# Performance work log

Hardware: AMD Instinct MI355X
Metric: run time of the kernel (lower is better)

The kernel has to match this reference:

```python
import jax, jax.numpy as jnp
import numpy as np

# D4 Daubechies filter taps (same filter replicated across all channels)
D4 = jnp.array([0.4829629131445341, 0.8365163037378079, 0.2241438680420134, -0.1294095225512604], dtype=jnp.float32)
N_SCALES = 11
SPARSE_DILATIONS = (512, 1024)


def setup_inputs() -> dict:
    key = jax.random.key(0)
    ks = jax.random.split(key, 12)
    B, N, D, H = 4, 4096, 1024, 16
    s = 0.02
    return {
        "x": jax.random.normal(ks[0], (B, N, D), dtype=jnp.float32),
        "Wqkv": jax.random.normal(ks[1], (D, 3 * D), dtype=jnp.float32) * s,
        "bqkv": jnp.zeros((3 * D,), dtype=jnp.float32),
        "Wout": jax.random.normal(ks[2], (D, D), dtype=jnp.float32) * s,
        "bout": jnp.zeros((D,), dtype=jnp.float32),
        "Wgate": jax.random.normal(ks[3], (D, D), dtype=jnp.float32) * s,
        "bgate": jnp.full((D,), 2.0, dtype=jnp.float32),  # nn.init.constant_(bias, 2.0)
        "scale_gain": jax.random.normal(ks[4], (N_SCALES, H), dtype=jnp.float32) * 0.1,
        "skip_w": jnp.full((len(SPARSE_DILATIONS),), -4.0, dtype=jnp.float32)
                  + jax.random.normal(ks[5], (len(SPARSE_DILATIONS),), dtype=jnp.float32) * 0.1,
        "coupling": jnp.eye(H, dtype=jnp.float32)
                    + 0.01 * jax.random.normal(ks[6], (H, H), dtype=jnp.float32),
    }


def _shift_right(t, s, N):
    """Causal shift along seq axis (axis=2): out[i] = t[i-s], zeros for i < s."""
    if s == 0:
        return t
    return jnp.pad(t, ((0, 0), (0, 0), (s, 0), (0, 0)))[:, :, :N, :]


def reference(x, Wqkv, bqkv, Wout, bout, Wgate, bgate, scale_gain, skip_w, coupling):
    B, N, D = x.shape
    H = scale_gain.shape[1]
    HD = D // H

    qkv = x @ Wqkv + bqkv                       # [B, N, 3D]
    q, k, v = jnp.split(qkv, 3, axis=-1)

    def to_heads(t):
        return t.reshape(B, N, H, HD).transpose(0, 2, 1, 3)  # [B, H, N, HD]

    q, k, v = to_heads(q), to_heads(k), to_heads(v)

    k_mag = jnp.linalg.norm(k, axis=-1, keepdims=True)       # [B, H, N, 1]
    field = v * k_mag                                        # [B, H, N, HD]

    # --- 11-scale causal D4 dilated depthwise conv pyramid ---
    # Depthwise conv with identical filter on every channel == weighted sum of
    # causally shifted copies: y[n] = sum_t D4[t] * field[n - (3-t)*d]
    gains = jax.nn.softmax(scale_gain, axis=0)               # [S, H]
    acc = jnp.zeros_like(field)
    for j in range(scale_gain.shape[0]):
        d = 1 << j
        y = sum(D4[t] * _shift_right(field, (3 - t) * d, N) for t in range(4))
        acc = acc + gains[j][None, :, None, None] * y
    field = acc

    # --- sparse long-distance causal skips (1-tap copies at d=512, 1024) ---
    sw = jax.nn.sigmoid(skip_w)
    skip = sum(sw[i] * _shift_right(field, d, N) for i, d in enumerate(SPARSE_DILATIONS))
    field = field + skip

    # --- gated field coupling across heads ---
    coup = jax.nn.softmax(coupling, axis=-1)                 # [H, H]
    field = jnp.einsum('ij,bjnd->bind', coup, field)

    q_flat = q.transpose(0, 2, 1, 3).reshape(B, N, D)
    gate = jax.nn.sigmoid(q_flat @ Wgate + bgate)
    gathered = field.transpose(0, 2, 1, 3).reshape(B, N, D)
    out = (gathered * gate) @ Wout + bout                    # dropout = identity (eval)
    return out
```

## Files before the change

kernel.cpp:

```cpp
#include <hip/hip_runtime.h>
#include <hip/hip_bf16.h>
#include <math.h>

#define BB 4
#define NSEQ 4096
#define DD 1024
#define HH 16
#define HD 64
#define MROWS (BB * NSEQ)

typedef __attribute__((ext_vector_type(8))) short short8;
typedef float v4f __attribute__((ext_vector_type(4)));
typedef unsigned short u16;

typedef __attribute__((address_space(1))) const void gconst_void;
typedef __attribute__((address_space(3))) void lds_void_t;

__device__ __constant__ int SHIFTS[24] = {0,1,2,3,4,6,8,12,16,24,32,48,64,96,128,192,256,384,512,768,1024,1536,2048,3072};

__device__ inline u16 f2bf(float f) {
    unsigned u = __float_as_uint(f);
    unsigned r = u + 0x7fffu + ((u >> 16) & 1u);
    return (u16)(r >> 16);
}
__device__ inline float bf2f(u16 h) {
    return __uint_as_float(((unsigned)h) << 16);
}
__device__ inline void gl2lds16(const u16* g, u16* l) {
    __builtin_amdgcn_global_load_lds((gconst_void*)g, (lds_void_t*)l, 16, 0, 0);
}

__global__ void prep_kernel(const float* __restrict__ scale_gain, const float* __restrict__ skip_w,
                            const float* __restrict__ coupling, float* __restrict__ coefTab,
                            float* __restrict__ coupS, float* __restrict__ swbuf) {
    const float D4T[4] = {0.4829629131445341f, 0.8365163037378079f, 0.2241438680420134f, -0.1294095225512604f};
    int t = threadIdx.x;
    if (t < 2) swbuf[t] = 1.0f / (1.0f + expf(-skip_w[t]));
    if (t < 16) {
        float m = -1e30f;
        for (int j = 0; j < 16; j++) m = fmaxf(m, coupling[t * 16 + j]);
        float s = 0.f, e[16];
        for (int j = 0; j < 16; j++) { e[j] = expf(coupling[t * 16 + j] - m); s += e[j]; }
        for (int j = 0; j < 16; j++) coupS[t * 16 + j] = e[j] / s;
        float g[11];
        m = -1e30f;
        for (int j = 0; j < 11; j++) m = fmaxf(m, scale_gain[j * 16 + t]);
        s = 0.f;
        for (int j = 0; j < 11; j++) { g[j] = expf(scale_gain[j * 16 + t] - m); s += g[j]; }
        for (int j = 0; j < 11; j++) g[j] /= s;
        float cf[24];
        for (int i = 0; i < 24; i++) cf[i] = 0.f;
        for (int j = 0; j < 11; j++) {
            int d = 1 << j;
            for (int tt = 0; tt < 4; tt++) {
                int sh = (3 - tt) * d;
                for (int i = 0; i < 24; i++) {
                    if (SHIFTS[i] == sh) { cf[i] += g[j] * D4T[tt]; break; }
                }
            }
        }
        for (int i = 0; i < 24; i++) coefTab[t * 24 + i] = cf[i];
    }
}

__global__ __launch_bounds__(256) void bfuse_kernel(const float* __restrict__ bqkv, const float* __restrict__ Wgate,
                                                    const float* __restrict__ bgate, float* __restrict__ bfuse) {
    __shared__ float part[4][64];
    int nloc = threadIdx.x & 63, strip = threadIdx.x >> 6;
    int n = blockIdx.x * 64 + nloc;
    float s = 0.f;
    for (int j = strip * 256; j < strip * 256 + 256; j++)
        s += bqkv[j] * Wgate[(long)j * 1024 + n];
    part[strip][nloc] = s;
    __syncthreads();
    if (strip == 0)
        bfuse[n] = bgate[n] + part[0][nloc] + part[1][nloc] + part[2][nloc] + part[3][nloc];
}

__global__ __launch_bounds__(256) void cast_x_kernel(const float* __restrict__ x, u16* __restrict__ xb) {
    long i = ((long)blockIdx.x * 256 + threadIdx.x) * 8;
    float4 f0 = *(const float4*)&x[i];
    float4 f1 = *(const float4*)&x[i + 4];
    u16 o[8];
    o[0] = f2bf(f0.x); o[1] = f2bf(f0.y); o[2] = f2bf(f0.z); o[3] = f2bf(f0.w);
    o[4] = f2bf(f1.x); o[5] = f2bf(f1.y); o[6] = f2bf(f1.z); o[7] = f2bf(f1.w);
    *(uint4*)&xb[i] = *(uint4*)o;
}

__global__ __launch_bounds__(256) void transpose_cast(const float* __restrict__ W, long ldw,
                                                      u16* __restrict__ WT, long ldt) {
    __shared__ float tile[32][33];
    int tx = threadIdx.x, ty = threadIdx.y;
    long x = (long)blockIdx.x * 32 + tx;
    long y0 = (long)blockIdx.y * 32;
    for (int r = 0; r < 32; r += 8)
        tile[ty + r][tx] = W[(y0 + ty + r) * ldw + x];
    __syncthreads();
    for (int r = 0; r < 32; r += 8)
        WT[((long)blockIdx.x * 32 + ty + r) * ldt + y0 + tx] = f2bf(tile[tx][ty + r]);
}

__global__ __launch_bounds__(256) void cast_q_kernel(const float* __restrict__ Wqkv, u16* __restrict__ WqC) {
    long i = ((long)blockIdx.x * 256 + threadIdx.x) * 4;
    int row = (int)(i >> 10);
    int col = (int)(i & 1023);
    float4 f = *(const float4*)&Wqkv[(long)row * 3072 + col];
    ushort4 o;
    o.x = f2bf(f.x); o.y = f2bf(f.y); o.z = f2bf(f.z); o.w = f2bf(f.w);
    *(ushort4*)&WqC[i] = o;
}

__global__ __launch_bounds__(256) void gemm64(const u16* __restrict__ A, long lda,
                                              const u16* __restrict__ BT, long ldb, int K,
                                              u16* __restrict__ C, long ldc) {
    __shared__ u16 As[64 * 32];
    __shared__ u16 Bs[64 * 32];
    const int tid = threadIdx.x;
    const int wv = tid >> 6, lane = tid & 63;
    const int wm = wv >> 1, wn = wv & 1;
    const int lrow = lane & 15, kq = lane >> 4;
    const long m0 = (long)blockIdx.y * 64, n0 = (long)blockIdx.x * 64;

    const int srow = wv * 16 + (lane >> 2);
    const int scol = ((lane & 3) ^ ((lane >> 3) & 3)) * 8;
    const u16* gA = A + (m0 + srow) * lda + scol;
    const u16* gB = BT + (n0 + srow) * ldb + scol;
    u16* la = &As[wv * 16 * 32];
    u16* lb = &Bs[wv * 16 * 32];

    const int acol = (kq ^ ((lrow >> 1) & 3)) * 8;
    v4f acc[2][2];
#pragma unroll
    for (int i = 0; i < 2; i++)
#pragma unroll
        for (int j = 0; j < 2; j++) acc[i][j] = (v4f){0.f, 0.f, 0.f, 0.f};

    for (int k0 = 0; k0 < K; k0 += 32) {
        gl2lds16(gA + k0, la);
        gl2lds16(gB + k0, lb);
        __syncthreads();
        short8 af[2], bf[2];
#pragma unroll
        for (int i = 0; i < 2; i++) af[i] = *(const short8*)&As[(wm * 32 + i * 16 + lrow) * 32 + acol];
#pragma unroll
        for (int j = 0; j < 2; j++) bf[j] = *(const short8*)&Bs[(wn * 32 + j * 16 + lrow) * 32 + acol];
#pragma unroll
        for (int im = 0; im < 2; im++)
#pragma unroll
            for (int in = 0; in < 2; in++)
                acc[im][in] = __builtin_amdgcn_mfma_f32_16x16x32_bf16(af[im], bf[in], acc[im][in], 0, 0, 0);
        __syncthreads();
    }
#pragma unroll
    for (int im = 0; im < 2; im++) {
#pragma unroll
        for (int in = 0; in < 2; in++) {
            long row = m0 + wm * 32 + im * 16 + kq * 4;
            long col = n0 + wn * 32 + in * 16 + lrow;
#pragma unroll
            for (int i = 0; i < 4; i++)
                C[(row + i) * ldc + col] = f2bf(acc[im][in][i]);
        }
    }
}

#define WAITV(N) asm volatile("s_waitcnt vmcnt(" #N ")" ::: "memory")

template <int CMODE>
__global__ __launch_bounds__(512, 2) void gemm256(const u16* __restrict__ A, long lda,
                                                  const u16* __restrict__ BT, long ldb, int K,
                                                  const float* __restrict__ bias,
                                                  const float* __restrict__ bias2,
                                                  void* __restrict__ C0, void* __restrict__ C1,
                                                  long ldc, float* __restrict__ kmagOut) {
    __shared__ u16 smem[4 * 2 * 8192];
    const int tid = threadIdx.x;
    const int wv = tid >> 6, lane = tid & 63;
    const int wm = wv >> 2, wn = wv & 3;
    const int lrow = lane & 15, kq = lane >> 4;
    const long m0 = (long)blockIdx.y * 256, n0 = (long)blockIdx.x * 256;

    const int srow = wv * 32 + (lane >> 2);
    const int scol = ((lane & 3) ^ ((lane >> 3) & 3)) * 8;
    const u16* gA0 = A + (m0 + srow) * lda + scol;
    const u16* gA1 = gA0 + 16 * lda;
    const u16* gB0 = BT + (n0 + srow) * ldb + scol;
    const u16* gB1 = gB0 + 16 * ldb;
    const int sb = wv * 32 * 32;

    const int acol = (kq ^ ((lrow >> 1) & 3)) * 8;
    const int aoff = (wm * 128 + lrow) * 32 + acol;
    const int boff = (wn * 64 + lrow) * 32 + acol;

    v4f acc[8][4];
#pragma unroll
    for (int i = 0; i < 8; i++)
#pragma unroll
        for (int j = 0; j < 4; j++) acc[i][j] = (v4f){0.f, 0.f, 0.f, 0.f};

    const int NT = K >> 5;

#define STAGE256(tt) {                                              \
        const int _kk = (tt) << 5;                                  \
        u16* _p = &smem[(((tt) & 3) * 2) * 8192 + sb];              \
        gl2lds16(gA0 + _kk, _p);                                    \
        gl2lds16(gA1 + _kk, _p + 512);                              \
        gl2lds16(gB0 + _kk, _p + 8192);                             \
        gl2lds16(gB1 + _kk, _p + 8192 + 512); }

    STAGE256(0)
    STAGE256(1)
    STAGE256(2)
    WAITV(8);
    __builtin_amdgcn_s_barrier();

    for (int t = 0; t < NT; ++t) {
        if (t + 3 < NT) STAGE256(t + 3)
        const u16* Ab = &smem[((t & 3) * 2) * 8192];
        const u16* Bb = Ab + 8192;
        short8 af[8], bf[4];
#pragma unroll
        for (int i = 0; i < 8; i++) af[i] = *(const short8*)&Ab[aoff + i * 512];
#pragma unroll
        for (int j = 0; j < 4; j++) bf[j] = *(const short8*)&Bb[boff + j * 512];
        __builtin_amdgcn_s_setprio(1);
#pragma unroll
        for (int i = 0; i < 8; i++)
#pragma unroll
            for (int j = 0; j < 4; j++)
                acc[i][j] = __builtin_amdgcn_mfma_f32_16x16x32_bf16(af[i], bf[j], acc[i][j], 0, 0, 0);
        __builtin_amdgcn_s_setprio(0);
        if (t + 3 < NT)      { WAITV(8); }
        else if (t + 2 < NT) { WAITV(4); }
        else if (t + 1 < NT) { WAITV(0); }
        __builtin_amdgcn_s_barrier();
    }
#undef STAGE256

    if (CMODE == 0) {
        float* C = (float*)C0;
#pragma unroll
        for (int im = 0; im < 8; im++) {
#pragma unroll
            for (int in = 0; in < 4; in++) {
                long row = m0 + wm * 128 + im * 16 + kq * 4;
                long col = n0 + wn * 64 + in * 16 + lrow;
                float bv = bias ? bias[col] : 0.f;
#pragma unroll
                for (int i = 0; i < 4; i++)
                    C[(row + i) * ldc + col] = acc[im][in][i] + bv;
            }
        }
    } else {
        u16* kvC = (u16*)C0;
        u16* gateC = (u16*)C1;
        const bool isGate = (n0 >= 2048);
        if (isGate) {
#pragma unroll
            for (int im = 0; im < 8; im++) {
#pragma unroll
                for (int in = 0; in < 4; in++) {
                    long row = m0 + wm * 128 + im * 16 + kq * 4;
                    long gc = n0 + wn * 64 + in * 16 + lrow - 2048;
                    float bv = bias2[gc];
#pragma unroll
                    for (int i = 0; i < 4; i++) {
                        float sgm = 1.0f / (1.0f + expf(-(acc[im][in][i] + bv)));
                        gateC[(row + i) * 1024 + gc] = f2bf(sgm);
                    }
                }
            }
        } else if (n0 < 1024) {
            float bvv[4];
#pragma unroll
            for (int in = 0; in < 4; in++) bvv[in] = bias[n0 + wn * 64 + in * 16 + lrow];
            const int h_g = (int)(n0 >> 6) + wn;
#pragma unroll
            for (int im = 0; im < 8; im++) {
                long row = m0 + wm * 128 + im * 16 + kq * 4;
                float ss0 = 0.f, ss1 = 0.f, ss2 = 0.f, ss3 = 0.f;
#pragma unroll
                for (int in = 0; in < 4; in++) {
                    long col = n0 + wn * 64 + in * 16 + lrow;
                    float v0 = acc[im][in][0] + bvv[in];
                    float v1 = acc[im][in][1] + bvv[in];
                    float v2 = acc[im][in][2] + bvv[in];
                    float v3 = acc[im][in][3] + bvv[in];
                    kvC[(row + 0) * 2048 + col] = f2bf(v0);
                    kvC[(row + 1) * 2048 + col] = f2bf(v1);
                    kvC[(row + 2) * 2048 + col] = f2bf(v2);
                    kvC[(row + 3) * 2048 + col] = f2bf(v3);
                    ss0 += v0 * v0; ss1 += v1 * v1; ss2 += v2 * v2; ss3 += v3 * v3;
                }
#pragma unroll
                for (int m = 1; m <= 8; m <<= 1) {
                    ss0 += __shfl_xor(ss0, m, 64);
                    ss1 += __shfl_xor(ss1, m, 64);
                    ss2 += __shfl_xor(ss2, m, 64);
                    ss3 += __shfl_xor(ss3, m, 64);
                }
                if (lrow == 0) {
                    int b = (int)(row >> 12);
                    int n = (int)(row & 4095);
                    float4 o4 = make_float4(sqrtf(ss0), sqrtf(ss1), sqrtf(ss2), sqrtf(ss3));
                    *(float4*)&kmagOut[((long)b * HH + h_g) * NSEQ + n] = o4;
                }
            }
        } else {
#pragma unroll
            for (int im = 0; im < 8; im++) {
#pragma unroll
                for (int in = 0; in < 4; in++) {
                    long row = m0 + wm * 128 + im * 16 + kq * 4;
                    long col = n0 + wn * 64 + in * 16 + lrow;
                    float bv = bias[col];
#pragma unroll
                    for (int i = 0; i < 4; i++)
                        kvC[(row + i) * 2048 + col] = f2bf(acc[im][in][i] + bv);
                }
            }
        }
    }
}

__global__ __launch_bounds__(256) void foldv_kernel(const u16* __restrict__ kv,
                                                    const float* __restrict__ kmag,
                                                    u16* __restrict__ field_t) {
    __shared__ u16 tile[64][72];
    int bh = blockIdx.y;
    int n0 = blockIdx.x * 64;
    int b = bh >> 4, h = bh & 15;
    int t = threadIdx.x;

    {
        int r = t >> 2;
        int c0 = (t & 3) * 16;
        int n = n0 + r;
        const u16* src = kv + ((long)(b * NSEQ + n)) * 2048 + 1024 + h * 64 + c0;
        uint4 u0 = *(const uint4*)src;
        uint4 u1 = *(const uint4*)(src + 8);
        float km = kmag[(long)bh * NSEQ + n];
        u16 in[16], o[16];
        *(uint4*)&in[0] = u0;
        *(uint4*)&in[8] = u1;
#pragma unroll
        for (int i = 0; i < 16; i++) o[i] = f2bf(bf2f(in[i]) * km);
        *(uint4*)&tile[r][c0] = *(uint4*)&o[0];
        *(uint4*)&tile[r][c0 + 8] = *(uint4*)&o[8];
    }
    __syncthreads();

    {
        int cg = t >> 4;
        int q = t & 15;
        u16 o[16];
#pragma unroll
        for (int j = 0; j < 4; j++) {
            int r = q * 4 + j;
            *(ushort4*)&o[j * 4] = *(const ushort4*)&tile[r][cg * 4];
        }
        u16* dst = field_t + (((long)bh * 16 + cg) * NSEQ + n0 + q * 4) * 4;
        *(uint4*)&dst[0] = *(uint4*)&o[0];
        *(uint4*)&dst[8] = *(uint4*)&o[8];
    }
}

__global__ __launch_bounds__(512) void pyramid_kernel(const u16* __restrict__ field_t,
                                                      const float* __restrict__ coefTab,
                                                      const float* __restrict__ swbuf,
                                                      u16* __restrict__ accp) {
    __shared__ u16 lds4[NSEQ * 4];
    int blk = blockIdx.x;
    int bh = blk >> 4;
    int cg = blk & 15;
    int hd0 = cg * 4;
    int h = bh & 15;
    int tid = threadIdx.x;

    float cf[24];
#pragma unroll
    for (int i = 0; i < 24; i++) cf[i] = coefTab[h * 24 + i];
    float sw0 = swbuf[0], sw1 = swbuf[1];

    const u16* src = field_t + ((long)bh * 16 + cg) * NSEQ * 4;
#pragma unroll
    for (int k = 0; k < 4; k++) {
        long e = ((long)k * 512 + tid) * 8;
        *(uint4*)&lds4[e] = *(const uint4*)&src[e];
    }
    __syncthreads();

    u16* dst = accp + (long)bh * NSEQ * HD + hd0;
    float p1x = 0.f, p1y = 0.f, p1z = 0.f, p1w = 0.f;
    float p2x = 0.f, p2y = 0.f, p2z = 0.f, p2w = 0.f;
    for (int i = 0; i < 8; i++) {
        int n = tid + i * 512;
        float ax = 0.f, ay = 0.f, az = 0.f, aw = 0.f;
#pragma unroll
        for (int tp = 0; tp < 24; tp++) {
            int s = SHIFTS[tp];
            if (n >= s) {
                const ushort4 f = *(const ushort4*)&lds4[(n - s) * 4];
                float c = cf[tp];
                ax += c * bf2f(f.x); ay += c * bf2f(f.y);
                az += c * bf2f(f.z); aw += c * bf2f(f.w);
            }
        }
        float ox = ax + sw0 * p1x + sw1 * p2x;
        float oy = ay + sw0 * p1y + sw1 * p2y;
        float oz = az + sw0 * p1z + sw1 * p2z;
        float ow = aw + sw0 * p1w + sw1 * p2w;
        ushort4 o;
        o.x = f2bf(ox); o.y = f2bf(oy); o.z = f2bf(oz); o.w = f2bf(ow);
        *(ushort4*)&dst[(long)n * HD] = o;
        p2x = p1x; p2y = p1y; p2z = p1z; p2w = p1w;
        p1x = ax;  p1y = ay;  p1z = az;  p1w = aw;
    }
}

__global__ __launch_bounds__(256) void couple_kernel(const u16* __restrict__ accp,
                                                     const u16* __restrict__ gate,
                                                     const float* __restrict__ coupS,
                                                     u16* __restrict__ A3) {
    __shared__ float tmp[DD];
    __shared__ float cp[256];
    int row = blockIdx.x;
    int b = row >> 12;
    int n = row & 4095;
    int tid = threadIdx.x;
    cp[tid] = coupS[tid];

    int e = tid * 4;
    int j = e >> 6;
    int hd = e & 63;
    const u16* base = accp + (((long)b * HH + j) * NSEQ + n) * HD + hd;
    ushort4 v0 = *(const ushort4*)base;
    tmp[e] = bf2f(v0.x); tmp[e + 1] = bf2f(v0.y);
    tmp[e + 2] = bf2f(v0.z); tmp[e + 3] = bf2f(v0.w);
    __syncthreads();

    float ox = 0.f, oy = 0.f, oz = 0.f, ow = 0.f;
#pragma unroll
    for (int jj = 0; jj < 16; jj++) {
        float c = cp[j * 16 + jj];
        ox += c * tmp[jj * 64 + hd];
        oy += c * tmp[jj * 64 + hd + 1];
        oz += c * tmp[jj * 64 + hd + 2];
        ow += c * tmp[jj * 64 + hd + 3];
    }
    const ushort4 g = *(const ushort4*)&gate[(long)row * DD + e];
    ox *= bf2f(g.x); oy *= bf2f(g.y); oz *= bf2f(g.z); ow *= bf2f(g.w);
    ushort4 o;
    o.x = f2bf(ox); o.y = f2bf(oy); o.z = f2bf(oz); o.w = f2bf(ow);
    *(ushort4*)&A3[(long)row * DD + e] = o;
}

extern "C" void kernel_launch(void* const* d_in, const int* in_sizes, int n_in,
                              void* d_out, int out_size, void* d_ws, size_t ws_size,
                              hipStream_t stream) {
    const float* x        = (const float*)d_in[0];
    const float* Wqkv     = (const float*)d_in[1];
    const float* bqkv     = (const float*)d_in[2];
    const float* Wout     = (const float*)d_in[3];
    const float* bout     = (const float*)d_in[4];
    const float* Wgate    = (const float*)d_in[5];
    const float* bgate    = (const float*)d_in[6];
    const float* scale_g  = (const float*)d_in[7];
    const float* skip_w   = (const float*)d_in[8];
    const float* coupling = (const float*)d_in[9];

    char* ws = (char*)d_ws;
    size_t off = 0;
    auto alloc = [&](size_t bytes) { char* p = ws + off; off += (bytes + 255) & ~(size_t)255; return p; };

    u16*   kv      = (u16*)alloc((size_t)MROWS * 2048 * 2);
    u16*   gate    = (u16*)alloc((size_t)MROWS * DD * 2);
    u16*   field_t = (u16*)alloc((size_t)BB * HH * NSEQ * HD * 2);
    u16*   WkvT    = (u16*)alloc((size_t)2048 * 1024 * 2);
    u16*   WfuseT  = (u16*)alloc((size_t)1024 * 1024 * 2);
    u16*   WgateT  = (u16*)alloc((size_t)1024 * 1024 * 2);
    u16*   WoutT   = (u16*)alloc((size_t)1024 * 1024 * 2);
    u16*   WqC     = (u16*)alloc((size_t)1024 * 1024 * 2);
    float* kmag    = (float*)alloc((size_t)BB * HH * NSEQ * 4);
    float* bfuse   = (float*)alloc(1024 * 4);
    float* coefT   = (float*)alloc(16 * 24 * 4);
    float* coupS   = (float*)alloc(256 * 4);
    float* swbuf   = (float*)alloc(2 * 4);
    u16*   xb   = field_t;
    u16*   accp = kv;
    u16*   A3   = kv + (size_t)BB * HH * NSEQ * HD;

    cast_x_kernel<<<(MROWS * DD) / (256 * 8), 256, 0, stream>>>(x, xb);

    prep_kernel<<<1, 64, 0, stream>>>(scale_g, skip_w, coupling, coefT, coupS, swbuf);
    bfuse_kernel<<<16, 256, 0, stream>>>(bqkv, Wgate, bgate, bfuse);

    transpose_cast<<<dim3(64, 32), dim3(32, 8), 0, stream>>>(Wqkv + 1024, 3072, WkvT, 1024);
    transpose_cast<<<dim3(32, 32), dim3(32, 8), 0, stream>>>(Wgate, 1024, WgateT, 1024);
    transpose_cast<<<dim3(32, 32), dim3(32, 8), 0, stream>>>(Wout, 1024, WoutT, 1024);
    cast_q_kernel<<<1024, 256, 0, stream>>>(Wqkv, WqC);

    gemm64<<<dim3(16, 16), 256, 0, stream>>>(WgateT, 1024, WqC, 1024, 1024, WfuseT, 1024);

    gemm256<2><<<dim3(12, 64), 512, 0, stream>>>(xb, 1024, WkvT, 1024, 1024,
                                                 bqkv + 1024, bfuse, kv, gate, 0, kmag);

    foldv_kernel<<<dim3(64, 64), 256, 0, stream>>>(kv, kmag, field_t);

    pyramid_kernel<<<BB * HH * 16, 512, 0, stream>>>(field_t, coefT, swbuf, accp);

    couple_kernel<<<MROWS, 256, 0, stream>>>(accp, gate, coupS, A3);

    gemm256<0><<<dim3(4, 64), 512, 0, stream>>>(A3, 1024, WoutT, 1024, 1024,
                                                bout, (const float*)nullptr, (float*)d_out, nullptr,
                                                1024, (float*)nullptr);
}
```

Baseline: 458.1 us.

## Split GEMM main loop into two barrier-synchronized half-phases interleaving loads and MFMAs

Restructures the 256x256 GEMM inner loop into two phases. Each phase reads half the A fragments from LDS, issues half of the next stage's global-to-LDS copies (A, then B), barriers, then runs half the MFMAs. This is a ping-pong style schedule meant to spread memory issue across the iteration and overlap it with matrix math across the two co-resident workgroups. It adds two extra barriers and lgkmcnt waits per iteration, which could add stalls.

```diff
diff --git a/kernel.cpp b/kernel.cpp
--- a/kernel.cpp
+++ b/kernel.cpp
@@ -165,6 +165,7 @@
 }
 
 #define WAITV(N) asm volatile("s_waitcnt vmcnt(" #N ")" ::: "memory")
+#define LGKM0()  asm volatile("s_waitcnt lgkmcnt(0)" ::: "memory")
 
 template <int CMODE>
 __global__ __launch_bounds__(512, 2) void gemm256(const u16* __restrict__ A, long lda,
@@ -200,32 +201,50 @@
 
     const int NT = K >> 5;
 
-#define STAGE256(tt) {                                              \
+#define STAGE_A(tt) {                                               \
         const int _kk = (tt) << 5;                                  \
         u16* _p = &smem[(((tt) & 3) * 2) * 8192 + sb];              \
         gl2lds16(gA0 + _kk, _p);                                    \
-        gl2lds16(gA1 + _kk, _p + 512);                              \
+        gl2lds16(gA1 + _kk, _p + 512); }
+#define STAGE_B(tt) {                                               \
+        const int _kk = (tt) << 5;                                  \
+        u16* _p = &smem[(((tt) & 3) * 2) * 8192 + sb];              \
         gl2lds16(gB0 + _kk, _p + 8192);                             \
         gl2lds16(gB1 + _kk, _p + 8192 + 512); }
 
-    STAGE256(0)
-    STAGE256(1)
-    STAGE256(2)
+    STAGE_A(0) STAGE_B(0)
+    STAGE_A(1) STAGE_B(1)
+    STAGE_A(2) STAGE_B(2)
     WAITV(8);
     __builtin_amdgcn_s_barrier();
 
     for (int t = 0; t < NT; ++t) {
-        if (t + 3 < NT) STAGE256(t + 3)
         const u16* Ab = &smem[((t & 3) * 2) * 8192];
         const u16* Bb = Ab + 8192;
         short8 af[8], bf[4];
 #pragma unroll
-        for (int i = 0; i < 8; i++) af[i] = *(const short8*)&Ab[aoff + i * 512];
+        for (int i = 0; i < 4; i++) af[i] = *(const short8*)&Ab[aoff + i * 512];
 #pragma unroll
         for (int j = 0; j < 4; j++) bf[j] = *(const short8*)&Bb[boff + j * 512];
+        if (t + 3 < NT) STAGE_A(t + 3)
+        __builtin_amdgcn_s_barrier();
+        LGKM0();
         __builtin_amdgcn_s_setprio(1);
 #pragma unroll
-        for (int i = 0; i < 8; i++)
+        for (int i = 0; i < 4; i++)
+#pragma unroll
+            for (int j = 0; j < 4; j++)
+                acc[i][j] = __builtin_amdgcn_mfma_f32_16x16x32_bf16(af[i], bf[j], acc[i][j], 0, 0, 0);
+        __builtin_amdgcn_s_setprio(0);
+        __builtin_amdgcn_s_barrier();
+#pragma unroll
+        for (int i = 4; i < 8; i++) af[i] = *(const short8*)&Ab[aoff + i * 512];
+        if (t + 3 < NT) STAGE_B(t + 3)
+        __builtin_amdgcn_s_barrier();
+        LGKM0();
+        __builtin_amdgcn_s_setprio(1);
+#pragma unroll
+        for (int i = 4; i < 8; i++)
 #pragma unroll
             for (int j = 0; j < 4; j++)
                 acc[i][j] = __builtin_amdgcn_mfma_f32_16x16x32_bf16(af[i], bf[j], acc[i][j], 0, 0, 0);
@@ -235,7 +254,8 @@
         else if (t + 1 < NT) { WAITV(0); }
         __builtin_amdgcn_s_barrier();
     }
-#undef STAGE256
+#undef STAGE_A
+#undef STAGE_B
 
     if (CMODE == 0) {
         float* C = (float*)C0;
```

After: 451.4 us. About the same (-1.5%).

## Merge preprocessing kernels into one launch and swizzle gemm256 block order

Applied to the files above, without the earlier changes.

Seven small preprocessing launches (x cast, weight transposes, Wq cast, bias fusion, softmax/coef prep) are merged into one kernel that dispatches on block index, which removes launch gaps and tail idle time between them. gemm256 also remaps its linear block id so that consecutive workgroups are spread in strides of eight across the grid. The remap is meant to match how the scheduler distributes workgroups across XCDs so each die's L2 sees better A/B tile reuse. The merged kernel carries branch divergence per block and keeps a __syncthreads inside a device helper reached only by some blocks.

```diff
diff --git a/kernel.cpp b/kernel.cpp
--- a/kernel.cpp
+++ b/kernel.cpp
@@ -30,84 +30,99 @@
     __builtin_amdgcn_global_load_lds((gconst_void*)g, (lds_void_t*)l, 16, 0, 0);
 }
 
-__global__ void prep_kernel(const float* __restrict__ scale_gain, const float* __restrict__ skip_w,
-                            const float* __restrict__ coupling, float* __restrict__ coefTab,
-                            float* __restrict__ coupS, float* __restrict__ swbuf) {
-    const float D4T[4] = {0.4829629131445341f, 0.8365163037378079f, 0.2241438680420134f, -0.1294095225512604f};
-    int t = threadIdx.x;
-    if (t < 2) swbuf[t] = 1.0f / (1.0f + expf(-skip_w[t]));
-    if (t < 16) {
-        float m = -1e30f;
-        for (int j = 0; j < 16; j++) m = fmaxf(m, coupling[t * 16 + j]);
-        float s = 0.f, e[16];
-        for (int j = 0; j < 16; j++) { e[j] = expf(coupling[t * 16 + j] - m); s += e[j]; }
-        for (int j = 0; j < 16; j++) coupS[t * 16 + j] = e[j] / s;
-        float g[11];
-        m = -1e30f;
-        for (int j = 0; j < 11; j++) m = fmaxf(m, scale_gain[j * 16 + t]);
-        s = 0.f;
-        for (int j = 0; j < 11; j++) { g[j] = expf(scale_gain[j * 16 + t] - m); s += g[j]; }
-        for (int j = 0; j < 11; j++) g[j] /= s;
-        float cf[24];
-        for (int i = 0; i < 24; i++) cf[i] = 0.f;
-        for (int j = 0; j < 11; j++) {
-            int d = 1 << j;
-            for (int tt = 0; tt < 4; tt++) {
-                int sh = (3 - tt) * d;
-                for (int i = 0; i < 24; i++) {
-                    if (SHIFTS[i] == sh) { cf[i] += g[j] * D4T[tt]; break; }
+__device__ inline void tcast_dev(const float* __restrict__ W, long ldw, u16* __restrict__ WT, long ldt,
+                                 int bx, int by, int tx, int ty, float (*tile)[33]) {
+    long xg = (long)bx * 32 + tx;
+    long y0 = (long)by * 32;
+    for (int r = 0; r < 32; r += 8)
+        tile[ty + r][tx] = W[(y0 + ty + r) * ldw + xg];
+    __syncthreads();
+    for (int r = 0; r < 32; r += 8)
+        WT[((long)bx * 32 + ty + r) * ldt + y0 + tx] = f2bf(tile[tx][ty + r]);
+}
+
+__global__ __launch_bounds__(256) void prep_data_kernel(
+    const float* __restrict__ x, const float* __restrict__ Wqkv,
+    const float* __restrict__ Wgate, const float* __restrict__ Wout,
+    const float* __restrict__ bqkv, const float* __restrict__ bgate,
+    const float* __restrict__ scale_gain, const float* __restrict__ skip_w,
+    const float* __restrict__ coupling,
+    u16* __restrict__ xb, u16* __restrict__ WkvT, u16* __restrict__ WgateT,
+    u16* __restrict__ WoutT, u16* __restrict__ WqC,
+    float* __restrict__ bfuse, float* __restrict__ coefTab,
+    float* __restrict__ coupS, float* __restrict__ swbuf) {
+    __shared__ float tile[32][33];
+    __shared__ float part[4][64];
+    const int bid = blockIdx.x;
+    const int t = threadIdx.x;
+    const int tx = t & 31, ty = t >> 5;
+
+    if (bid < 8192) {
+        long i = ((long)bid * 256 + t) * 8;
+        float4 f0 = *(const float4*)&x[i];
+        float4 f1 = *(const float4*)&x[i + 4];
+        u16 o[8];
+        o[0] = f2bf(f0.x); o[1] = f2bf(f0.y); o[2] = f2bf(f0.z); o[3] = f2bf(f0.w);
+        o[4] = f2bf(f1.x); o[5] = f2bf(f1.y); o[6] = f2bf(f1.z); o[7] = f2bf(f1.w);
+        *(uint4*)&xb[i] = *(uint4*)o;
+    } else if (bid < 10240) {
+        int r = bid - 8192;
+        tcast_dev(Wqkv + 1024, 3072, WkvT, 1024, r & 63, r >> 6, tx, ty, tile);
+    } else if (bid < 11264) {
+        int r = bid - 10240;
+        tcast_dev(Wgate, 1024, WgateT, 1024, r & 31, r >> 5, tx, ty, tile);
+    } else if (bid < 12288) {
+        int r = bid - 11264;
+        tcast_dev(Wout, 1024, WoutT, 1024, r & 31, r >> 5, tx, ty, tile);
+    } else if (bid < 13312) {
+        int r = bid - 12288;
+        long i = ((long)r * 256 + t) * 4;
+        int row = (int)(i >> 10);
+        int col = (int)(i & 1023);
+        float4 f = *(const float4*)&Wqkv[(long)row * 3072 + col];
+        ushort4 o;
+        o.x = f2bf(f.x); o.y = f2bf(f.y); o.z = f2bf(f.z); o.w = f2bf(f.w);
+        *(ushort4*)&WqC[i] = o;
+    } else if (bid < 13328) {
+        int r = bid - 13312;
+        int nloc = t & 63, strip = t >> 6;
+        int n = r * 64 + nloc;
+        float s = 0.f;
+        for (int j = strip * 256; j < strip * 256 + 256; j++)
+            s += bqkv[j] * Wgate[(long)j * 1024 + n];
+        part[strip][nloc] = s;
+        __syncthreads();
+        if (strip == 0)
+            bfuse[n] = bgate[n] + part[0][nloc] + part[1][nloc] + part[2][nloc] + part[3][nloc];
+    } else {
+        const float D4T[4] = {0.4829629131445341f, 0.8365163037378079f, 0.2241438680420134f, -0.1294095225512604f};
+        if (t < 2) swbuf[t] = 1.0f / (1.0f + expf(-skip_w[t]));
+        if (t < 16) {
+            float m = -1e30f;
+            for (int j = 0; j < 16; j++) m = fmaxf(m, coupling[t * 16 + j]);
+            float s = 0.f, e[16];
+            for (int j = 0; j < 16; j++) { e[j] = expf(coupling[t * 16 + j] - m); s += e[j]; }
+            for (int j = 0; j < 16; j++) coupS[t * 16 + j] = e[j] / s;
+            float g[11];
+            m = -1e30f;
+            for (int j = 0; j < 11; j++) m = fmaxf(m, scale_gain[j * 16 + t]);
+            s = 0.f;
+            for (int j = 0; j < 11; j++) { g[j] = expf(scale_gain[j * 16 + t] - m); s += g[j]; }
+            for (int j = 0; j < 11; j++) g[j] /= s;
+            float cf[24];
+            for (int i = 0; i < 24; i++) cf[i] = 0.f;
+            for (int j = 0; j < 11; j++) {
+                int d = 1 << j;
+                for (int tt = 0; tt < 4; tt++) {
+                    int sh = (3 - tt) * d;
+                    for (int i = 0; i < 24; i++) {
+                        if (SHIFTS[i] == sh) { cf[i] += g[j] * D4T[tt]; break; }
+                    }
                 }
             }
+            for (int i = 0; i < 24; i++) coefTab[t * 24 + i] = cf[i];
         }
-        for (int i = 0; i < 24; i++) coefTab[t * 24 + i] = cf[i];
-    }
-}
-
-__global__ __launch_bounds__(256) void bfuse_kernel(const float* __restrict__ bqkv, const float* __restrict__ Wgate,
-                                                    const float* __restrict__ bgate, float* __restrict__ bfuse) {
-    __shared__ float part[4][64];
-    int nloc = threadIdx.x & 63, strip = threadIdx.x >> 6;
-    int n = blockIdx.x * 64 + nloc;
-    float s = 0.f;
-    for (int j = strip * 256; j < strip * 256 + 256; j++)
-        s += bqkv[j] * Wgate[(long)j * 1024 + n];
-    part[strip][nloc] = s;
-    __syncthreads();
-    if (strip == 0)
-        bfuse[n] = bgate[n] + part[0][nloc] + part[1][nloc] + part[2][nloc] + part[3][nloc];
-}
-
-__global__ __launch_bounds__(256) void cast_x_kernel(const float* __restrict__ x, u16* __restrict__ xb) {
-    long i = ((long)blockIdx.x * 256 + threadIdx.x) * 8;
-    float4 f0 = *(const float4*)&x[i];
-    float4 f1 = *(const float4*)&x[i + 4];
-    u16 o[8];
-    o[0] = f2bf(f0.x); o[1] = f2bf(f0.y); o[2] = f2bf(f0.z); o[3] = f2bf(f0.w);
-    o[4] = f2bf(f1.x); o[5] = f2bf(f1.y); o[6] = f2bf(f1.z); o[7] = f2bf(f1.w);
-    *(uint4*)&xb[i] = *(uint4*)o;
-}
-
-__global__ __launch_bounds__(256) void transpose_cast(const float* __restrict__ W, long ldw,
-                                                      u16* __restrict__ WT, long ldt) {
-    __shared__ float tile[32][33];
-    int tx = threadIdx.x, ty = threadIdx.y;
-    long x = (long)blockIdx.x * 32 + tx;
-    long y0 = (long)blockIdx.y * 32;
-    for (int r = 0; r < 32; r += 8)
-        tile[ty + r][tx] = W[(y0 + ty + r) * ldw + x];
-    __syncthreads();
-    for (int r = 0; r < 32; r += 8)
-        WT[((long)blockIdx.x * 32 + ty + r) * ldt + y0 + tx] = f2bf(tile[tx][ty + r]);
-}
-
-__global__ __launch_bounds__(256) void cast_q_kernel(const float* __restrict__ Wqkv, u16* __restrict__ WqC) {
-    long i = ((long)blockIdx.x * 256 + threadIdx.x) * 4;
-    int row = (int)(i >> 10);
-    int col = (int)(i & 1023);
-    float4 f = *(const float4*)&Wqkv[(long)row * 3072 + col];
-    ushort4 o;
-    o.x = f2bf(f.x); o.y = f2bf(f.y); o.z = f2bf(f.z); o.w = f2bf(f.w);
-    *(ushort4*)&WqC[i] = o;
+    }
 }
 
 __global__ __launch_bounds__(256) void gemm64(const u16* __restrict__ A, long lda,
@@ -178,7 +193,12 @@
     const int wv = tid >> 6, lane = tid & 63;
     const int wm = wv >> 2, wn = wv & 3;
     const int lrow = lane & 15, kq = lane >> 4;
-    const long m0 = (long)blockIdx.y * 256, n0 = (long)blockIdx.x * 256;
+
+    const int nwg = gridDim.x * gridDim.y;
+    const int lbid = blockIdx.y * gridDim.x + blockIdx.x;
+    const int swz = (lbid & 7) * (nwg >> 3) + (lbid >> 3);
+    const int bx = swz % gridDim.x, by = swz / gridDim.x;
+    const long m0 = (long)by * 256, n0 = (long)bx * 256;
 
     const int srow = wv * 32 + (lane >> 2);
     const int scol = ((lane & 3) ^ ((lane >> 3) & 3)) * 8;
@@ -490,15 +510,10 @@
     u16*   accp = kv;
     u16*   A3   = kv + (size_t)BB * HH * NSEQ * HD;
 
-    cast_x_kernel<<<(MROWS * DD) / (256 * 8), 256, 0, stream>>>(x, xb);
-
-    prep_kernel<<<1, 64, 0, stream>>>(scale_g, skip_w, coupling, coefT, coupS, swbuf);
-    bfuse_kernel<<<16, 256, 0, stream>>>(bqkv, Wgate, bgate, bfuse);
-
-    transpose_cast<<<dim3(64, 32), dim3(32, 8), 0, stream>>>(Wqkv + 1024, 3072, WkvT, 1024);
-    transpose_cast<<<dim3(32, 32), dim3(32, 8), 0, stream>>>(Wgate, 1024, WgateT, 1024);
-    transpose_cast<<<dim3(32, 32), dim3(32, 8), 0, stream>>>(Wout, 1024, WoutT, 1024);
-    cast_q_kernel<<<1024, 256, 0, stream>>>(Wqkv, WqC);
+    prep_data_kernel<<<13329, 256, 0, stream>>>(x, Wqkv, Wgate, Wout, bqkv, bgate,
+                                                scale_g, skip_w, coupling,
+                                                xb, WkvT, WgateT, WoutT, WqC,
+                                                bfuse, coefT, coupS, swbuf);
 
     gemm64<<<dim3(16, 16), 256, 0, stream>>>(WgateT, 1024, WqC, 1024, 1024, WfuseT, 1024);
 
```

New measurement: 432.3 us. 1.06x faster.
